# Kernel tuning notes

Measured on AMD Instinct MI355X. Metric: run time of the kernel, lower is better.

The kernel has to match this reference:

```python
import jax, jax.numpy as jnp
import numpy as np
from math import exp, log

# Instant-NGP style multi-hash-grid constants (match init_kwargs)
BASE_RES = 16
MAX_RES = 2048
N_GRIDS = 16
LOG2_T = 19
TABLE_SIZE = 1 << LOG2_T  # power of two -> mod == low-bit mask
FEAT = 2
N_POINTS = 1_000_000

_pls = exp((log(MAX_RES) - log(BASE_RES)) / (N_GRIDS - 1))
RESOLUTIONS = np.floor(np.array([BASE_RES * _pls ** i for i in range(N_GRIDS)])).astype(np.float32)
# 8 voxel corner offsets, i-major (i*4 + j*2 + k) like the torch VOXEL_VTX_OFFSET
OFFSETS = np.array([[i, j, k] for i in (0, 1) for j in (0, 1) for k in (0, 1)], dtype=np.int32)
PRIMES = np.array([1, 2654435761, 805459861], dtype=np.uint32)


def setup_inputs() -> dict:
    key = jax.random.key(0)
    k1, k2 = jax.random.split(key)
    x = jax.random.normal(k1, (N_POINTS, 3), dtype=jnp.float32)
    # nn.init.uniform_(weight, a=-1e-4, b=1e-4)
    tables = jax.random.uniform(k2, (N_GRIDS, TABLE_SIZE, FEAT),
                                minval=-1e-4, maxval=1e-4, dtype=jnp.float32)
    return {"x": x, "tables": tables}


def _forward(x, tables):
    inbox = jnp.all((x >= -1.0) & (x <= 1.0), axis=-1)  # [B]
    offs = jnp.asarray(OFFSETS)                          # [8,3]
    primes = jnp.asarray(PRIMES)                         # [3] uint32
    res = jnp.asarray(RESOLUTIONS)                       # [G]
    # torch computes x_normed / interp weights under no_grad -> no grad to x
    xs = jax.lax.stop_gradient(x)

    def level(table, r):
        # (x - bbox_min) / (bbox_max - bbox_min) * resolution, bbox = [-1,1]^3
        xn = (xs + 1.0) * 0.5 * r                        # [B,3]
        v0 = jnp.floor(xn).astype(jnp.int32)             # [B,3]
        w = xn - v0.astype(jnp.float32)                  # [B,3] trilerp weights
        vidx = (v0[:, None, :] + offs[None]).astype(jnp.uint32)  # [B,8,3]
        # prime-XOR spatial hash; uint32 wraparound matches torch int64 math
        # modulo the power-of-two table size (low bits identical)
        h = (vidx[..., 0] * primes[0]) ^ (vidx[..., 1] * primes[1]) ^ (vidx[..., 2] * primes[2])
        h = (h & jnp.uint32(TABLE_SIZE - 1)).astype(jnp.int32)   # [B,8]
        feats = table[h]                                  # [B,8,F] gather
        # corner (i,j,k) weight = prod over dims of (w if bit else 1-w)
        wgt = jnp.prod(jnp.where(offs[None] == 1, w[:, None, :], 1.0 - w[:, None, :]), axis=-1)  # [B,8]
        c = jnp.einsum('bc,bcf->bf', wgt, feats)          # [B,F]
        return jnp.where(inbox[:, None], c, 0.0)          # out-of-bbox -> zeros

    per_level = jax.vmap(level)(tables, res)              # [G,B,F]
    B = x.shape[0]
    return jnp.transpose(per_level, (1, 0, 2)).reshape(B, N_GRIDS * FEAT)


def reference(x, tables):
    return _forward(x, tables)
```

## Files before the change

### kernel.cpp

```cpp
#include <hip/hip_runtime.h>
#include <hip/hip_bf16.h>
#include <math.h>

#define N_POINTS 1000000
#define N_GRIDS  16
#define LOG2_T   19
#define TABLE_MASK ((1u << LOG2_T) - 1u)
#define NBLOCKS  ((N_POINTS + 255) / 256)
#define CONV_BLOCKS 4096
#define FUSED_BLOCKS 2048
#define TAILB_BLOCKS 4096
#define N_ENTRIES (N_GRIDS << LOG2_T)
#define NCELL_AX 32
#define N_CELLS  (NCELL_AX * NCELL_AX * NCELL_AX)

struct ResArr { float r[N_GRIDS]; };

__device__ __forceinline__ unsigned pack_bf16x2(float a, float b)
{
    __hip_bfloat16 ha = __float2bfloat16(a);
    __hip_bfloat16 hb = __float2bfloat16(b);
    unsigned short ua = *(unsigned short*)&ha;
    unsigned short ub = *(unsigned short*)&hb;
    return (unsigned)ua | ((unsigned)ub << 16);
}

__device__ __forceinline__ float2 unpack_bf16x2(unsigned v)
{
    unsigned lo = (v & 0xffffu) << 16;
    unsigned hi = v & 0xffff0000u;
    return make_float2(__uint_as_float(lo), __uint_as_float(hi));
}

__device__ __forceinline__ unsigned expand_bits(unsigned v)
{
    v &= 0x3ffu;
    v = (v | (v << 16)) & 0x30000FFu;
    v = (v | (v << 8))  & 0x300F00Fu;
    v = (v | (v << 4))  & 0x30C30C3u;
    v = (v | (v << 2))  & 0x9249249u;
    return v;
}

__device__ __forceinline__ int morton_cell(float x0, float x1, float x2)
{
    int cx = (int)floorf((x0 + 1.f) * 16.f);
    int cy = (int)floorf((x1 + 1.f) * 16.f);
    int cz = (int)floorf((x2 + 1.f) * 16.f);
    cx = min(NCELL_AX - 1, max(0, cx));
    cy = min(NCELL_AX - 1, max(0, cy));
    cz = min(NCELL_AX - 1, max(0, cz));
    return (int)((expand_bits((unsigned)cx) << 2) |
                 (expand_bits((unsigned)cy) << 1) |
                  expand_bits((unsigned)cz));
}

__device__ __forceinline__ void gather_level_bf16(
    float x0, float x1, float x2, float r,
    const unsigned* __restrict__ tbl, float& c0, float& c1)
{
    const float xn0 = (x0 + 1.0f) * 0.5f * r;
    const float xn1 = (x1 + 1.0f) * 0.5f * r;
    const float xn2 = (x2 + 1.0f) * 0.5f * r;
    const float f0 = floorf(xn0), f1 = floorf(xn1), f2 = floorf(xn2);
    const unsigned v0 = (unsigned)(int)f0;
    const unsigned v1 = (unsigned)(int)f1;
    const unsigned v2 = (unsigned)(int)f2;
    const float w0 = xn0 - f0, w1 = xn1 - f1, w2 = xn2 - f2;

    unsigned fv[8];
    #pragma unroll
    for (int k = 0; k < 8; ++k) {
        const unsigned vx = v0 + ((k >> 2) & 1);
        const unsigned vy = v1 + ((k >> 1) & 1);
        const unsigned vz = v2 + (k & 1);
        unsigned h = vx ^ (vy * 2654435761u) ^ (vz * 805459861u);
        fv[k] = tbl[h & TABLE_MASK];
    }
    c0 = 0.f; c1 = 0.f;
    #pragma unroll
    for (int k = 0; k < 8; ++k) {
        const float wgt = ((k & 4) ? w0 : 1.0f - w0) *
                          ((k & 2) ? w1 : 1.0f - w1) *
                          ((k & 1) ? w2 : 1.0f - w2);
        const float2 f = unpack_bf16x2(fv[k]);
        c0 += wgt * f.x;
        c1 += wgt * f.y;
    }
}

__global__ __launch_bounds__(256)
void hist_kernel(const float* __restrict__ x, int* __restrict__ rank,
                 unsigned* __restrict__ hist)
{
    const int p = blockIdx.x * 256 + threadIdx.x;
    if (p >= N_POINTS) return;
    const float x0 = x[3 * p], x1 = x[3 * p + 1], x2 = x[3 * p + 2];
    const bool inbox = (x0 >= -1.f) & (x0 <= 1.f) &
                       (x1 >= -1.f) & (x1 <= 1.f) &
                       (x2 >= -1.f) & (x2 <= 1.f);
    if (inbox) {
        const int cell = morton_cell(x0, x1, x2);
        atomicAdd(&hist[cell], 1u);
        rank[p] = cell;
    } else {
        rank[p] = -1;
    }
}

__global__ __launch_bounds__(1024)
void scan_kernel(unsigned* __restrict__ hist, unsigned* __restrict__ counter)
{
    __shared__ unsigned partial[1024];
    const int tid = threadIdx.x;
    const int base = tid * (N_CELLS / 1024);
    unsigned v[N_CELLS / 1024];
    unsigned s = 0;
    #pragma unroll
    for (int i = 0; i < N_CELLS / 1024; ++i) { v[i] = hist[base + i]; s += v[i]; }
    partial[tid] = s;
    __syncthreads();
    for (int off = 1; off < 1024; off <<= 1) {
        unsigned t = (tid >= off) ? partial[tid - off] : 0u;
        __syncthreads();
        partial[tid] += t;
        __syncthreads();
    }
    if (tid == 1023) counter[0] = partial[1023];
    unsigned run = partial[tid] - s;
    #pragma unroll
    for (int i = 0; i < N_CELLS / 1024; ++i) {
        const unsigned c = v[i];
        hist[base + i] = run;
        run += c;
    }
}

__global__ __launch_bounds__(256)
void scatter_conv_kernel(const float* __restrict__ tables,
                         unsigned* __restrict__ tb,
                         const float* __restrict__ x, int* __restrict__ rank,
                         float4* __restrict__ xw, unsigned* __restrict__ hist)
{
    if (blockIdx.x < CONV_BLOCKS) {
        const unsigned nthr = CONV_BLOCKS * 256;
        for (unsigned e4 = blockIdx.x * 256 + threadIdx.x; e4 < (N_ENTRIES / 4);
             e4 += nthr) {
            const float4 a = ((const float4*)tables)[2 * e4];
            const float4 b = ((const float4*)tables)[2 * e4 + 1];
            uint4 o;
            o.x = pack_bf16x2(a.x, a.y);
            o.y = pack_bf16x2(a.z, a.w);
            o.z = pack_bf16x2(b.x, b.y);
            o.w = pack_bf16x2(b.z, b.w);
            ((uint4*)tb)[e4] = o;
        }
    } else {
        const int p = (blockIdx.x - CONV_BLOCKS) * 256 + threadIdx.x;
        if (p >= N_POINTS) return;
        const int cell = rank[p];
        if (cell < 0) return;
        const unsigned rk = atomicAdd(&hist[cell], 1u);
        rank[p] = (int)rk;
        xw[rk] = make_float4(x[3 * p], x[3 * p + 1], x[3 * p + 2],
                             __int_as_float(p));
    }
}

__global__ __launch_bounds__(256)
void fused_levels_kernel(const float4* __restrict__ xw,
                         const unsigned* __restrict__ counter,
                         const unsigned* __restrict__ tb,
                         unsigned* __restrict__ ws2, ResArr res)
{
    const unsigned k    = blockIdx.x & 7;
    const unsigned bix  = blockIdx.x >> 3;
    const unsigned nbx  = gridDim.x >> 3;
    const unsigned cnt  = *counter;
    const unsigned per  = (cnt + nbx - 1) / nbx;
    const unsigned lo   = bix * per;
    const unsigned hi   = min(cnt, lo + per);

    #pragma unroll 1
    for (int t = 0; t < 2; ++t) {
        const int g = t ? (15 - (int)k) : (int)k;
        const float r = res.r[g];
        const unsigned* __restrict__ tbl = tb + ((size_t)g << LOG2_T);
        unsigned* __restrict__ wrow = ws2 + (size_t)g * N_POINTS;
        for (unsigned i = lo + threadIdx.x; i < hi; i += 256) {
            const float4 v = xw[i];
            float c0, c1;
            gather_level_bf16(v.x, v.y, v.z, r, tbl, c0, c1);
            wrow[i] = pack_bf16x2(c0, c1);
        }
    }
}

__global__ __launch_bounds__(256)
void tail_kernel(const int* __restrict__ rank, const float4* __restrict__ xw,
                 const unsigned* __restrict__ counter,
                 const unsigned* __restrict__ ws2, float* __restrict__ out)
{
    const int t = threadIdx.x;
    if (blockIdx.x < NBLOCKS) {
        const int P0 = blockIdx.x * 256;
        float4* __restrict__ out4 = (float4*)out + (size_t)P0 * 8;
        const float4 z = make_float4(0.f, 0.f, 0.f, 0.f);
        #pragma unroll
        for (int i = 0; i < 8; ++i) {
            const int j  = i * 256 + t;
            const int pp = P0 + (j >> 3);
            if (pp < N_POINTS && rank[pp] < 0) out4[j] = z;
        }
    } else {
        const unsigned cnt = *counter;
        const unsigned tot = cnt * 8u;
        const unsigned bix = blockIdx.x - NBLOCKS;
        for (unsigned tg = bix * 256 + t; tg < tot; tg += TAILB_BLOCKS * 256) {
            const unsigned i = tg >> 3, q = tg & 7;
            const unsigned a = ws2[(size_t)(2 * q) * N_POINTS + i];
            const unsigned b = ws2[(size_t)(2 * q + 1) * N_POINTS + i];
            const int p = __float_as_int(xw[i].w);
            const float2 fa = unpack_bf16x2(a);
            const float2 fb = unpack_bf16x2(b);
            ((float4*)out)[(size_t)p * 8 + q] =
                make_float4(fa.x, fa.y, fb.x, fb.y);
        }
    }
}

__device__ __forceinline__ void gather_level_f32(
    float x0, float x1, float x2, float r,
    const float2* __restrict__ tbl, float& c0, float& c1)
{
    const float xn0 = (x0 + 1.0f) * 0.5f * r;
    const float xn1 = (x1 + 1.0f) * 0.5f * r;
    const float xn2 = (x2 + 1.0f) * 0.5f * r;
    const float f0 = floorf(xn0), f1 = floorf(xn1), f2 = floorf(xn2);
    const unsigned v0 = (unsigned)(int)f0;
    const unsigned v1 = (unsigned)(int)f1;
    const unsigned v2 = (unsigned)(int)f2;
    const float w0 = xn0 - f0, w1 = xn1 - f1, w2 = xn2 - f2;
    c0 = 0.f; c1 = 0.f;
    #pragma unroll
    for (int k = 0; k < 8; ++k) {
        const unsigned vx = v0 + ((k >> 2) & 1);
        const unsigned vy = v1 + ((k >> 1) & 1);
        const unsigned vz = v2 + (k & 1);
        unsigned h = (vx * 1u) ^ (vy * 2654435761u) ^ (vz * 805459861u);
        h &= TABLE_MASK;
        const float wgt = ((k & 4) ? w0 : 1.0f - w0) *
                          ((k & 2) ? w1 : 1.0f - w1) *
                          ((k & 1) ? w2 : 1.0f - w2);
        const float2 f = tbl[h];
        c0 += wgt * f.x;
        c1 += wgt * f.y;
    }
}

__global__ __launch_bounds__(256)
void mono_kernel(const float* __restrict__ x, const float* __restrict__ tables,
                 float* __restrict__ out, ResArr res)
{
    int idx = blockIdx.x * blockDim.x + threadIdx.x;
    if (idx >= N_POINTS * N_GRIDS) return;
    int b = idx >> 4, g = idx & 15;
    float x0 = x[b * 3], x1 = x[b * 3 + 1], x2 = x[b * 3 + 2];
    bool inbox = (x0 >= -1.f) & (x0 <= 1.f) & (x1 >= -1.f) & (x1 <= 1.f) &
                 (x2 >= -1.f) & (x2 <= 1.f);
    float c0 = 0.f, c1 = 0.f;
    if (inbox) {
        const float2* tbl = (const float2*)tables + ((size_t)g << LOG2_T);
        gather_level_f32(x0, x1, x2, res.r[g], tbl, c0, c1);
    }
    ((float2*)out)[(size_t)b * N_GRIDS + g] = make_float2(c0, c1);
}

extern "C" void kernel_launch(void* const* d_in, const int* in_sizes, int n_in,
                              void* d_out, int out_size, void* d_ws, size_t ws_size,
                              hipStream_t stream)
{
    const float* x      = (const float*)d_in[0];
    const float* tables = (const float*)d_in[1];
    float* out          = (float*)d_out;

    ResArr res;
    double pls = exp((log(2048.0) - log(16.0)) / 15.0);
    for (int i = 0; i < N_GRIDS; ++i)
        res.r[i] = (float)floor(16.0 * pow(pls, (double)i));

    const size_t off_hist = 256;
    const size_t off_rank = off_hist + (size_t)N_CELLS * 4;
    const size_t off_xw   = off_rank + (size_t)N_POINTS * 4;
    const size_t off_ws2  = off_xw + (size_t)N_POINTS * 16;
    const size_t off_tb   = off_ws2 + (size_t)N_GRIDS * N_POINTS * 4;
    const size_t ws_needed = off_tb + (size_t)N_ENTRIES * 4;

    if (ws_size < ws_needed) {
        int total = N_POINTS * N_GRIDS;
        mono_kernel<<<(total + 255) / 256, 256, 0, stream>>>(x, tables, out, res);
        return;
    }

    char* w = (char*)d_ws;
    unsigned* counter = (unsigned*)w;
    unsigned* hist    = (unsigned*)(w + off_hist);
    int*      rank    = (int*)(w + off_rank);
    float4*   xw      = (float4*)(w + off_xw);
    unsigned* ws2     = (unsigned*)(w + off_ws2);
    unsigned* tb      = (unsigned*)(w + off_tb);

    (void)hipMemsetAsync(w, 0, off_rank, stream);
    hist_kernel<<<NBLOCKS, 256, 0, stream>>>(x, rank, hist);
    scan_kernel<<<1, 1024, 0, stream>>>(hist, counter);
    scatter_conv_kernel<<<CONV_BLOCKS + NBLOCKS, 256, 0, stream>>>(
        tables, tb, x, rank, xw, hist);
    fused_levels_kernel<<<FUSED_BLOCKS, 256, 0, stream>>>(xw, counter, tb,
                                                          ws2, res);
    tail_kernel<<<NBLOCKS + TAILB_BLOCKS, 256, 0, stream>>>(rank, xw, counter,
                                                            ws2, out);
}
```

Before: 195.9 us.

## Rebalance level-to-XCD work assignment and vectorize histogram scan

The fused levels kernel now splits each of the 8 block groups' work over 16 level-slices. The first seven levels stay whole per group and the remaining nine levels are cut into eighths spread across groups. This is meant to keep each group's table working set cache-resident (blockIdx&7 likely maps to an XCD) while balancing per-group load. The scan kernel also loads and stores the histogram as uint4 instead of scalars. It adds more complex range bookkeeping per block.

```diff
diff --git a/kernel.cpp b/kernel.cpp
--- a/kernel.cpp
+++ b/kernel.cpp
@@ -113,11 +113,14 @@
 {
     __shared__ unsigned partial[1024];
     const int tid = threadIdx.x;
-    const int base = tid * (N_CELLS / 1024);
-    unsigned v[N_CELLS / 1024];
+    uint4* __restrict__ hp = (uint4*)hist + tid * 8;
+    uint4 vv[8];
     unsigned s = 0;
     #pragma unroll
-    for (int i = 0; i < N_CELLS / 1024; ++i) { v[i] = hist[base + i]; s += v[i]; }
+    for (int i = 0; i < 8; ++i) {
+        vv[i] = hp[i];
+        s += vv[i].x + vv[i].y + vv[i].z + vv[i].w;
+    }
     partial[tid] = s;
     __syncthreads();
     for (int off = 1; off < 1024; off <<= 1) {
@@ -129,10 +132,13 @@
     if (tid == 1023) counter[0] = partial[1023];
     unsigned run = partial[tid] - s;
     #pragma unroll
-    for (int i = 0; i < N_CELLS / 1024; ++i) {
-        const unsigned c = v[i];
-        hist[base + i] = run;
-        run += c;
+    for (int i = 0; i < 8; ++i) {
+        uint4 o;
+        o.x = run; run += vv[i].x;
+        o.y = run; run += vv[i].y;
+        o.z = run; run += vv[i].z;
+        o.w = run; run += vv[i].w;
+        hp[i] = o;
     }
 }
 
@@ -173,21 +179,42 @@
                          const unsigned* __restrict__ tb,
                          unsigned* __restrict__ ws2, ResArr res)
 {
-    const unsigned k    = blockIdx.x & 7;
-    const unsigned bix  = blockIdx.x >> 3;
-    const unsigned nbx  = gridDim.x >> 3;
-    const unsigned cnt  = *counter;
-    const unsigned per  = (cnt + nbx - 1) / nbx;
-    const unsigned lo   = bix * per;
-    const unsigned hi   = min(cnt, lo + per);
-
+    const unsigned k   = blockIdx.x & 7;
+    const unsigned bix = blockIdx.x >> 3;
+    const unsigned nbx = gridDim.x >> 3;
+    const unsigned cnt = *counter;
+
+    auto b8 = [&](unsigned e) {
+        return (unsigned)(((unsigned long long)e * cnt) >> 3);
+    };
+
+    const unsigned per = (2 * cnt + nbx - 1) / nbx;
+    const unsigned blo = bix * per;
+    const unsigned bhi = blo + per;
+
+    unsigned cum = 0;
     #pragma unroll 1
-    for (int t = 0; t < 2; ++t) {
-        const int g = t ? (15 - (int)k) : (int)k;
+    for (int tix = 0; tix < 16; ++tix) {
+        int g; unsigned e;
+        if (tix < 7) { g = tix; e = k; }
+        else {
+            const unsigned u = 9u * k + (unsigned)(tix - 7);
+            g = 7 + (int)(u >> 3);
+            e = u & 7u;
+        }
+        const unsigned lo = b8(e), hi = b8(e + 1);
+        const unsigned len = hi - lo;
+        const unsigned s0 = max(blo, cum);
+        const unsigned s1 = min(bhi, cum + len);
+        cum += len;
+        if (s0 >= s1) continue;
+
         const float r = res.r[g];
         const unsigned* __restrict__ tbl = tb + ((size_t)g << LOG2_T);
         unsigned* __restrict__ wrow = ws2 + (size_t)g * N_POINTS;
-        for (unsigned i = lo + threadIdx.x; i < hi; i += 256) {
+        const unsigned ilo = lo + (s0 - (cum - len));
+        const unsigned ihi = lo + (s1 - (cum - len));
+        for (unsigned i = ilo + threadIdx.x; i < ihi; i += 256) {
             const float4 v = xw[i];
             float c0, c1;
             gather_level_bf16(v.x, v.y, v.z, r, tbl, c0, c1);
```

New measurement: 207.7 us. 6.0% more time.

## Rebalance independent work across kernels and vectorize the histogram scan

Applied to the files above, without the earlier changes.

Moves the fp32-to-bf16 table conversion into the histogram kernel so it runs alongside point binning rather than alongside the scatter. Moves the zero-fill of out-of-box outputs into the fused level-gather launch so it overlaps the gathers, leaving the tail kernel to do only the scatter-back. The scan kernel now reads and writes the histogram with uint4 vector accesses. Launch count is unchanged; the aim is better overlap of independent work, at the cost of extra traffic competing with the memory-bound gather phase.

```diff
diff --git a/kernel.cpp b/kernel.cpp
--- a/kernel.cpp
+++ b/kernel.cpp
@@ -90,62 +90,29 @@
 }
 
 __global__ __launch_bounds__(256)
-void hist_kernel(const float* __restrict__ x, int* __restrict__ rank,
-                 unsigned* __restrict__ hist)
-{
-    const int p = blockIdx.x * 256 + threadIdx.x;
-    if (p >= N_POINTS) return;
-    const float x0 = x[3 * p], x1 = x[3 * p + 1], x2 = x[3 * p + 2];
-    const bool inbox = (x0 >= -1.f) & (x0 <= 1.f) &
-                       (x1 >= -1.f) & (x1 <= 1.f) &
-                       (x2 >= -1.f) & (x2 <= 1.f);
-    if (inbox) {
-        const int cell = morton_cell(x0, x1, x2);
-        atomicAdd(&hist[cell], 1u);
-        rank[p] = cell;
+void hist_conv_kernel(const float* __restrict__ x, int* __restrict__ rank,
+                      unsigned* __restrict__ hist,
+                      const float* __restrict__ tables,
+                      unsigned* __restrict__ tb)
+{
+    if (blockIdx.x < NBLOCKS) {
+        const int p = blockIdx.x * 256 + threadIdx.x;
+        if (p >= N_POINTS) return;
+        const float x0 = x[3 * p], x1 = x[3 * p + 1], x2 = x[3 * p + 2];
+        const bool inbox = (x0 >= -1.f) & (x0 <= 1.f) &
+                           (x1 >= -1.f) & (x1 <= 1.f) &
+                           (x2 >= -1.f) & (x2 <= 1.f);
+        if (inbox) {
+            const int cell = morton_cell(x0, x1, x2);
+            atomicAdd(&hist[cell], 1u);
+            rank[p] = cell;
+        } else {
+            rank[p] = -1;
+        }
     } else {
-        rank[p] = -1;
-    }
-}
-
-__global__ __launch_bounds__(1024)
-void scan_kernel(unsigned* __restrict__ hist, unsigned* __restrict__ counter)
-{
-    __shared__ unsigned partial[1024];
-    const int tid = threadIdx.x;
-    const int base = tid * (N_CELLS / 1024);
-    unsigned v[N_CELLS / 1024];
-    unsigned s = 0;
-    #pragma unroll
-    for (int i = 0; i < N_CELLS / 1024; ++i) { v[i] = hist[base + i]; s += v[i]; }
-    partial[tid] = s;
-    __syncthreads();
-    for (int off = 1; off < 1024; off <<= 1) {
-        unsigned t = (tid >= off) ? partial[tid - off] : 0u;
-        __syncthreads();
-        partial[tid] += t;
-        __syncthreads();
-    }
-    if (tid == 1023) counter[0] = partial[1023];
-    unsigned run = partial[tid] - s;
-    #pragma unroll
-    for (int i = 0; i < N_CELLS / 1024; ++i) {
-        const unsigned c = v[i];
-        hist[base + i] = run;
-        run += c;
-    }
-}
-
-__global__ __launch_bounds__(256)
-void scatter_conv_kernel(const float* __restrict__ tables,
-                         unsigned* __restrict__ tb,
-                         const float* __restrict__ x, int* __restrict__ rank,
-                         float4* __restrict__ xw, unsigned* __restrict__ hist)
-{
-    if (blockIdx.x < CONV_BLOCKS) {
         const unsigned nthr = CONV_BLOCKS * 256;
-        for (unsigned e4 = blockIdx.x * 256 + threadIdx.x; e4 < (N_ENTRIES / 4);
-             e4 += nthr) {
+        for (unsigned e4 = (blockIdx.x - NBLOCKS) * 256 + threadIdx.x;
+             e4 < (N_ENTRIES / 4); e4 += nthr) {
             const float4 a = ((const float4*)tables)[2 * e4];
             const float4 b = ((const float4*)tables)[2 * e4 + 1];
             uint4 o;
@@ -155,77 +122,120 @@
             o.w = pack_bf16x2(b.z, b.w);
             ((uint4*)tb)[e4] = o;
         }
-    } else {
-        const int p = (blockIdx.x - CONV_BLOCKS) * 256 + threadIdx.x;
-        if (p >= N_POINTS) return;
-        const int cell = rank[p];
-        if (cell < 0) return;
-        const unsigned rk = atomicAdd(&hist[cell], 1u);
-        rank[p] = (int)rk;
-        xw[rk] = make_float4(x[3 * p], x[3 * p + 1], x[3 * p + 2],
-                             __int_as_float(p));
-    }
+    }
+}
+
+__global__ __launch_bounds__(1024)
+void scan_kernel(unsigned* __restrict__ hist, unsigned* __restrict__ counter)
+{
+    __shared__ unsigned partial[1024];
+    const int tid = threadIdx.x;
+    uint4* __restrict__ hp = (uint4*)hist + tid * 8;
+    uint4 vv[8];
+    unsigned s = 0;
+    #pragma unroll
+    for (int i = 0; i < 8; ++i) {
+        vv[i] = hp[i];
+        s += vv[i].x + vv[i].y + vv[i].z + vv[i].w;
+    }
+    partial[tid] = s;
+    __syncthreads();
+    for (int off = 1; off < 1024; off <<= 1) {
+        unsigned t = (tid >= off) ? partial[tid - off] : 0u;
+        __syncthreads();
+        partial[tid] += t;
+        __syncthreads();
+    }
+    if (tid == 1023) counter[0] = partial[1023];
+    unsigned run = partial[tid] - s;
+    #pragma unroll
+    for (int i = 0; i < 8; ++i) {
+        uint4 o;
+        o.x = run; run += vv[i].x;
+        o.y = run; run += vv[i].y;
+        o.z = run; run += vv[i].z;
+        o.w = run; run += vv[i].w;
+        hp[i] = o;
+    }
+}
+
+__global__ __launch_bounds__(256)
+void scatter_kernel(const float* __restrict__ x, int* __restrict__ rank,
+                    float4* __restrict__ xw, unsigned* __restrict__ hist)
+{
+    const int p = blockIdx.x * 256 + threadIdx.x;
+    if (p >= N_POINTS) return;
+    const int cell = rank[p];
+    if (cell < 0) return;
+    const unsigned rk = atomicAdd(&hist[cell], 1u);
+    rank[p] = (int)rk;
+    xw[rk] = make_float4(x[3 * p], x[3 * p + 1], x[3 * p + 2],
+                         __int_as_float(p));
 }
 
 __global__ __launch_bounds__(256)
 void fused_levels_kernel(const float4* __restrict__ xw,
                          const unsigned* __restrict__ counter,
                          const unsigned* __restrict__ tb,
-                         unsigned* __restrict__ ws2, ResArr res)
-{
-    const unsigned k    = blockIdx.x & 7;
-    const unsigned bix  = blockIdx.x >> 3;
-    const unsigned nbx  = gridDim.x >> 3;
-    const unsigned cnt  = *counter;
-    const unsigned per  = (cnt + nbx - 1) / nbx;
-    const unsigned lo   = bix * per;
-    const unsigned hi   = min(cnt, lo + per);
-
-    #pragma unroll 1
-    for (int t = 0; t < 2; ++t) {
-        const int g = t ? (15 - (int)k) : (int)k;
-        const float r = res.r[g];
-        const unsigned* __restrict__ tbl = tb + ((size_t)g << LOG2_T);
-        unsigned* __restrict__ wrow = ws2 + (size_t)g * N_POINTS;
-        for (unsigned i = lo + threadIdx.x; i < hi; i += 256) {
-            const float4 v = xw[i];
-            float c0, c1;
-            gather_level_bf16(v.x, v.y, v.z, r, tbl, c0, c1);
-            wrow[i] = pack_bf16x2(c0, c1);
+                         unsigned* __restrict__ ws2, ResArr res,
+                         const int* __restrict__ rank,
+                         float* __restrict__ out)
+{
+    if (blockIdx.x < FUSED_BLOCKS) {
+        const unsigned k    = blockIdx.x & 7;
+        const unsigned bix  = blockIdx.x >> 3;
+        const unsigned nbx  = FUSED_BLOCKS >> 3;
+        const unsigned cnt  = *counter;
+        const unsigned per  = (cnt + nbx - 1) / nbx;
+        const unsigned lo   = bix * per;
+        const unsigned hi   = min(cnt, lo + per);
+
+        #pragma unroll 1
+        for (int t = 0; t < 2; ++t) {
+            const int g = t ? (15 - (int)k) : (int)k;
+            const float r = res.r[g];
+            const unsigned* __restrict__ tbl = tb + ((size_t)g << LOG2_T);
+            unsigned* __restrict__ wrow = ws2 + (size_t)g * N_POINTS;
+            for (unsigned i = lo + threadIdx.x; i < hi; i += 256) {
+                const float4 v = xw[i];
+                float c0, c1;
+                gather_level_bf16(v.x, v.y, v.z, r, tbl, c0, c1);
+                wrow[i] = pack_bf16x2(c0, c1);
+            }
         }
-    }
-}
-
-__global__ __launch_bounds__(256)
-void tail_kernel(const int* __restrict__ rank, const float4* __restrict__ xw,
-                 const unsigned* __restrict__ counter,
-                 const unsigned* __restrict__ ws2, float* __restrict__ out)
-{
-    const int t = threadIdx.x;
-    if (blockIdx.x < NBLOCKS) {
-        const int P0 = blockIdx.x * 256;
+    } else {
+        const unsigned zb = blockIdx.x - FUSED_BLOCKS;
+        const int P0 = (int)zb * 256;
         float4* __restrict__ out4 = (float4*)out + (size_t)P0 * 8;
         const float4 z = make_float4(0.f, 0.f, 0.f, 0.f);
+        const int t = threadIdx.x;
         #pragma unroll
         for (int i = 0; i < 8; ++i) {
             const int j  = i * 256 + t;
             const int pp = P0 + (j >> 3);
             if (pp < N_POINTS && rank[pp] < 0) out4[j] = z;
         }
-    } else {
-        const unsigned cnt = *counter;
-        const unsigned tot = cnt * 8u;
-        const unsigned bix = blockIdx.x - NBLOCKS;
-        for (unsigned tg = bix * 256 + t; tg < tot; tg += TAILB_BLOCKS * 256) {
-            const unsigned i = tg >> 3, q = tg & 7;
-            const unsigned a = ws2[(size_t)(2 * q) * N_POINTS + i];
-            const unsigned b = ws2[(size_t)(2 * q + 1) * N_POINTS + i];
-            const int p = __float_as_int(xw[i].w);
-            const float2 fa = unpack_bf16x2(a);
-            const float2 fb = unpack_bf16x2(b);
-            ((float4*)out)[(size_t)p * 8 + q] =
-                make_float4(fa.x, fa.y, fb.x, fb.y);
-        }
+    }
+}
+
+__global__ __launch_bounds__(256)
+void tail_kernel(const float4* __restrict__ xw,
+                 const unsigned* __restrict__ counter,
+                 const unsigned* __restrict__ ws2, float* __restrict__ out)
+{
+    const int t = threadIdx.x;
+    const unsigned cnt = *counter;
+    const unsigned tot = cnt * 8u;
+    for (unsigned tg = blockIdx.x * 256 + t; tg < tot;
+         tg += TAILB_BLOCKS * 256) {
+        const unsigned i = tg >> 3, q = tg & 7;
+        const unsigned a = ws2[(size_t)(2 * q) * N_POINTS + i];
+        const unsigned b = ws2[(size_t)(2 * q + 1) * N_POINTS + i];
+        const int p = __float_as_int(xw[i].w);
+        const float2 fa = unpack_bf16x2(a);
+        const float2 fb = unpack_bf16x2(b);
+        ((float4*)out)[(size_t)p * 8 + q] =
+            make_float4(fa.x, fa.y, fb.x, fb.y);
     }
 }
 
@@ -311,12 +321,11 @@
     unsigned* tb      = (unsigned*)(w + off_tb);
 
     (void)hipMemsetAsync(w, 0, off_rank, stream);
-    hist_kernel<<<NBLOCKS, 256, 0, stream>>>(x, rank, hist);
+    hist_conv_kernel<<<NBLOCKS + CONV_BLOCKS, 256, 0, stream>>>(
+        x, rank, hist, tables, tb);
     scan_kernel<<<1, 1024, 0, stream>>>(hist, counter);
-    scatter_conv_kernel<<<CONV_BLOCKS + NBLOCKS, 256, 0, stream>>>(
-        tables, tb, x, rank, xw, hist);
-    fused_levels_kernel<<<FUSED_BLOCKS, 256, 0, stream>>>(xw, counter, tb,
-                                                          ws2, res);
-    tail_kernel<<<NBLOCKS + TAILB_BLOCKS, 256, 0, stream>>>(rank, xw, counter,
-                                                            ws2, out);
-}
+    scatter_kernel<<<NBLOCKS, 256, 0, stream>>>(x, rank, xw, hist);
+    fused_levels_kernel<<<FUSED_BLOCKS + NBLOCKS, 256, 0, stream>>>(
+        xw, counter, tb, ws2, res, rank, out);
+    tail_kernel<<<TAILB_BLOCKS, 256, 0, stream>>>(xw, counter, ws2, out);
+}
```

New measurement: 198.4 us. No clear change (+1.3%).
